# Kernel tuning notes

Hardware: AMD Instinct MI355X
Metric: run time of the kernel (lower is better)

The kernel has to match this reference:

```python
import jax, jax.numpy as jnp
import numpy as np

D_MODEL = 1024
NHEAD = 16
HEAD_DIM = D_MODEL // NHEAD
D_FF = 4096
BIAS_HID = 8
EPS = 1e-5


def _pair_bias(m, w1, b1, w2, b2):
    # m: [B,S,S] -> bias [B,S,S,nhead] via per-scalar MLP 1->hid->nhead
    h = jax.nn.relu(m[..., None] * w1 + b1)          # [B,S,S,hid]
    return jnp.einsum('bxyh,hn->bxyn', h, w2) + b2   # [B,S,S,nhead]


def _layernorm(x, g, b):
    mu = jnp.mean(x, axis=-1, keepdims=True)
    var = jnp.mean(jnp.square(x - mu), axis=-1, keepdims=True)
    return (x - mu) * jax.lax.rsqrt(var + EPS) * g + b


def setup_inputs() -> dict:
    key = jax.random.key(0)
    ks = jax.random.split(key, 20)
    B, S = 4, 1024
    sc = 1.0 / np.sqrt(D_MODEL)
    inp = {
        'src': jax.random.normal(ks[0], (B, S, D_MODEL), jnp.float32),
        't_deltas': jax.random.uniform(ks[1], (B, S, S), jnp.float32),
        'dists': jax.random.uniform(ks[2], (B, S, S), jnp.float32),
        'Wq': jax.random.normal(ks[3], (D_MODEL, D_MODEL), jnp.float32) * sc,
        'bq': jnp.zeros((D_MODEL,), jnp.float32),
        'Wk': jax.random.normal(ks[4], (D_MODEL, D_MODEL), jnp.float32) * sc,
        'bk': jnp.zeros((D_MODEL,), jnp.float32),
        'Wv': jax.random.normal(ks[5], (D_MODEL, D_MODEL), jnp.float32) * sc,
        'bv': jnp.zeros((D_MODEL,), jnp.float32),
        'tb_w1': jax.random.normal(ks[6], (BIAS_HID,), jnp.float32),
        'tb_b1': jnp.zeros((BIAS_HID,), jnp.float32),
        'tb_w2': jax.random.normal(ks[7], (BIAS_HID, NHEAD), jnp.float32) * 0.3,
        'tb_b2': jnp.zeros((NHEAD,), jnp.float32),
        'db_w1': jax.random.normal(ks[8], (BIAS_HID,), jnp.float32),
        'db_b1': jnp.zeros((BIAS_HID,), jnp.float32),
        'db_w2': jax.random.normal(ks[9], (BIAS_HID, NHEAD), jnp.float32) * 0.3,
        'db_b2': jnp.zeros((NHEAD,), jnp.float32),
        'W1': jax.random.normal(ks[10], (D_MODEL, D_FF), jnp.float32) * sc,
        'b1': jnp.zeros((D_FF,), jnp.float32),
        'W2': jax.random.normal(ks[11], (D_FF, D_MODEL), jnp.float32) / np.sqrt(D_FF),
        'b2': jnp.zeros((D_MODEL,), jnp.float32),
        'g1': jnp.ones((D_MODEL,), jnp.float32),
        'beta1': jnp.zeros((D_MODEL,), jnp.float32),
        'g2': jnp.ones((D_MODEL,), jnp.float32),
        'beta2': jnp.zeros((D_MODEL,), jnp.float32),
    }
    return inp


def reference(src, t_deltas, dists, Wq, bq, Wk, bk, Wv, bv,
              tb_w1, tb_b1, tb_w2, tb_b2, db_w1, db_b1, db_w2, db_b2,
              W1, b1, W2, b2, g1, beta1, g2, beta2):
    B, S, _ = src.shape
    # QKV projections -> [B, H, S, hd]
    q = (src @ Wq + bq).reshape(B, S, NHEAD, HEAD_DIM).transpose(0, 2, 1, 3)
    k = (src @ Wk + bk).reshape(B, S, NHEAD, HEAD_DIM).transpose(0, 2, 1, 3)
    v = (src @ Wv + bv).reshape(B, S, NHEAD, HEAD_DIM).transpose(0, 2, 1, 3)
    # scores scaled by sqrt(d_model) (as in the original, not head_dim)
    scores = jnp.einsum('bhqd,bhkd->bhqk', q, k) / jnp.sqrt(jnp.float32(D_MODEL))
    bias = (_pair_bias(t_deltas, tb_w1, tb_b1, tb_w2, tb_b2)
            + _pair_bias(dists, db_w1, db_b1, db_w2, db_b2))  # [B,S,S,H]
    scores = scores + bias.transpose(0, 3, 1, 2)
    attn = jax.nn.softmax(scores, axis=-1)
    out = jnp.einsum('bhqk,bhkd->bhqd', attn, v)
    out = out.transpose(0, 2, 1, 3).reshape(B, S, D_MODEL)
    x = _layernorm(src + out, g1, beta1)
    ffn = jax.nn.relu(x @ W1 + b1) @ W2 + b2
    return _layernorm(x + ffn, g2, beta2)
```

## Files before the change

### kernel.cpp

```cpp
#include <hip/hip_runtime.h>

typedef __bf16 bf16x8 __attribute__((ext_vector_type(8)));
typedef float f32x4 __attribute__((ext_vector_type(4)));
typedef unsigned short u16;

__device__ __forceinline__ u16 f2bf(float f) {
  union { float f; unsigned u; } x; x.f = f;
  unsigned r = x.u + 0x7fffu + ((x.u >> 16) & 1u);
  return (u16)(r >> 16);
}
__device__ __forceinline__ float bf2f(u16 u) {
  union { unsigned u; float f; } x; x.u = ((unsigned)u) << 16;
  return x.f;
}
__device__ __forceinline__ void gl_lds16(const void* g, void* l) {
  __builtin_amdgcn_global_load_lds(
      (const __attribute__((address_space(1))) void*)g,
      (__attribute__((address_space(3))) void*)l, 16, 0, 0);
}

__global__ __launch_bounds__(256) void cvt_kernel(const float* __restrict__ in,
                                                  u16* __restrict__ out, int n4) {
  int i = blockIdx.x * 256 + threadIdx.x;
  if (i >= n4) return;
  float4 v = ((const float4*)in)[i];
  unsigned lo = (unsigned)f2bf(v.x) | ((unsigned)f2bf(v.y) << 16);
  unsigned hi = (unsigned)f2bf(v.z) | ((unsigned)f2bf(v.w) << 16);
  uint2 u; u.x = lo; u.y = hi;
  *(uint2*)&out[(size_t)i * 4] = u;
}

__global__ __launch_bounds__(256) void tconv_kernel(const float* __restrict__ in,
                                                    u16* __restrict__ out, int R, int C) {
  __shared__ float tile[32][33];
  int c0 = blockIdx.x * 32, r0 = blockIdx.y * 32;
  int tx = threadIdx.x & 31, ty = threadIdx.x >> 5;
#pragma unroll
  for (int i = 0; i < 4; i++)
    tile[ty + i * 8][tx] = in[(size_t)(r0 + ty + i * 8) * C + c0 + tx];
  __syncthreads();
#pragma unroll
  for (int i = 0; i < 4; i++)
    out[(size_t)(c0 + ty + i * 8) * R + r0 + tx] = f2bf(tile[tx][ty + i * 8]);
}

__global__ __launch_bounds__(256) void bcat_kernel(const float* __restrict__ bq,
                                                   const float* __restrict__ bk,
                                                   const float* __restrict__ bv,
                                                   float* __restrict__ o) {
  int i = blockIdx.x * 256 + threadIdx.x;
  if (i >= 3072) return;
  o[i] = i < 1024 ? bq[i] : (i < 2048 ? bk[i - 1024] : bv[i - 2048]);
}

template <int EPI>
__global__ __launch_bounds__(256) void gemm128_kernel(const u16* __restrict__ A,
                                                      const u16* __restrict__ Bt,
                                                      const float* __restrict__ bias,
                                                      void* __restrict__ out,
                                                      int M, int N, int K,
                                                      float qscale, int kslice) {
  __shared__ u16 lds[2][2][2][4096];
  int tid = threadIdx.x, w = tid >> 6, lane = tid & 63;
  int l16 = lane & 15, lhi = lane >> 4;
  int wr = w >> 1, wc = w & 1;
  int GX = gridDim.x;
  int nwg = GX * gridDim.y;
  int nlin = blockIdx.y * GX + blockIdx.x;
  int cpx = nwg >> 3;
  int sw = (nlin & 7) * cpx + (nlin >> 3);
  int m0 = (sw / GX) * 128, n0 = (sw % GX) * 128;
  int z = blockIdx.z;
  const u16* Ag = A + (size_t)m0 * K + z * kslice;
  const u16* Bg = Bt + (size_t)n0 * K + z * kslice;
  f32x4 acc[4][4] = {};
  int nt = kslice >> 6;

  int srow = tid >> 2;
  int sxor = ((tid & 3) ^ ((tid >> 3) & 3)) * 8;
  int rga = (lhi ^ ((l16 >> 1) & 3)) * 8;

  auto stageTK = [&](int buf, int kh, int t) {
    const u16* As = Ag + (size_t)t * 64 + kh * 32 + sxor;
    const u16* Bs = Bg + (size_t)t * 64 + kh * 32 + sxor;
#pragma unroll
    for (int ld = 0; ld < 2; ld++)
      gl_lds16(As + (size_t)(ld * 64 + srow) * K, &lds[buf][0][kh][ld * 2048 + w * 512]);
#pragma unroll
    for (int ld = 0; ld < 2; ld++)
      gl_lds16(Bs + (size_t)(ld * 64 + srow) * K, &lds[buf][1][kh][ld * 2048 + w * 512]);
  };
  auto rdAB = [&](int buf, int kh, bf16x8 (&af)[4], bf16x8 (&bfr)[4]) {
#pragma unroll
    for (int m = 0; m < 4; m++)
      af[m] = *(const bf16x8*)&lds[buf][0][kh][(wr * 64 + m * 16 + l16) * 32 + rga];
#pragma unroll
    for (int nn = 0; nn < 4; nn++)
      bfr[nn] = *(const bf16x8*)&lds[buf][1][kh][(wc * 64 + nn * 16 + l16) * 32 + rga];
  };
  auto mma16 = [&](bf16x8 (&af)[4], bf16x8 (&bfr)[4]) {
    __builtin_amdgcn_s_setprio(1);
#pragma unroll
    for (int m = 0; m < 4; m++)
#pragma unroll
      for (int nn = 0; nn < 4; nn++)
        acc[m][nn] =
            __builtin_amdgcn_mfma_f32_16x16x32_bf16(af[m], bfr[nn], acc[m][nn], 0, 0, 0);
    __builtin_amdgcn_s_setprio(0);
  };

  stageTK(0, 0, 0);
  stageTK(0, 1, 0);
  stageTK(1, 0, 1);

  for (int t = 0; t < nt; ++t) {
    int buf = t & 1, bufn = buf ^ 1;
    bool last = (t == nt - 1);
    bf16x8 af[4], bfr[4];
    if (!last) asm volatile("s_waitcnt vmcnt(8)" ::: "memory");
    else       asm volatile("s_waitcnt vmcnt(4)" ::: "memory");
    __builtin_amdgcn_s_barrier();
    rdAB(buf, 0, af, bfr);
    if (t + 1 < nt) stageTK(bufn, 1, t + 1);
    asm volatile("s_waitcnt lgkmcnt(0)" ::: "memory");
    __builtin_amdgcn_sched_barrier(0);
    mma16(af, bfr);
    if (!last) asm volatile("s_waitcnt vmcnt(8)" ::: "memory");
    else       asm volatile("s_waitcnt vmcnt(0)" ::: "memory");
    __builtin_amdgcn_s_barrier();
    rdAB(buf, 1, af, bfr);
    if (t + 2 < nt) stageTK(buf, 0, t + 2);
    asm volatile("s_waitcnt lgkmcnt(0)" ::: "memory");
    __builtin_amdgcn_sched_barrier(0);
    mma16(af, bfr);
  }

#pragma unroll
  for (int m = 0; m < 4; m++) {
    int gr = m0 + wr * 64 + m * 16 + lhi * 4;
#pragma unroll
    for (int nn = 0; nn < 4; nn++) {
      int gc = n0 + wc * 64 + nn * 16 + l16;
      float bv;
      if (EPI == 0 || EPI == 3) bv = (z == 0 && bias) ? bias[gc] : 0.f;
      else bv = bias[gc];
      if (EPI == 2) {
        int seg = gc >> 10, c = gc & 1023, h = c >> 6, d = c & 63;
        float sc = (seg == 0) ? qscale : 1.f;
#pragma unroll
        for (int r = 0; r < 4; r++) {
          int row = gr + r;
          int b = row >> 10, s = row & 1023;
          size_t idx = ((((size_t)seg * 4 + b) * 16 + h) * 1024 + s) * 64 + d;
          ((u16*)out)[idx] = f2bf((acc[m][nn][r] + bv) * sc);
        }
      } else if (EPI == 1) {
#pragma unroll
        for (int r = 0; r < 4; r++)
          ((u16*)out)[(size_t)(gr + r) * N + gc] = f2bf(fmaxf(acc[m][nn][r] + bv, 0.f));
      } else if (EPI == 3) {
#pragma unroll
        for (int r = 0; r < 4; r++)
          ((u16*)out)[(size_t)z * M * N + (size_t)(gr + r) * N + gc] = f2bf(acc[m][nn][r] + bv);
      } else {
#pragma unroll
        for (int r = 0; r < 4; r++)
          ((float*)out)[(size_t)z * M * N + (size_t)(gr + r) * N + gc] = acc[m][nn][r] + bv;
      }
    }
  }
}

__global__ __launch_bounds__(256) void vtrans_kernel(const u16* __restrict__ v,
                                                     u16* __restrict__ vt) {
  __shared__ u16 t[64][72];
  int bh = blockIdx.y, s0 = blockIdx.x * 64;
  int tid = threadIdx.x;
  int r = tid >> 2, c = (tid & 3) * 16;
  const u16* src = v + ((size_t)bh * 1024 + s0 + r) * 64 + c;
  *(int4*)&t[r][c] = *(const int4*)src;
  *(int4*)&t[r][c + 8] = *(const int4*)(src + 8);
  __syncthreads();
  int d = tid >> 2, sc = (tid & 3) * 16;
  u16 tmp[16];
#pragma unroll
  for (int j = 0; j < 16; j++) tmp[j] = t[sc + j][d];
  u16* dst = vt + ((size_t)bh * 64 + d) * 1024 + s0 + sc;
  *(int4*)dst = *(int4*)&tmp[0];
  *(int4*)(dst + 8) = *(int4*)&tmp[8];
}

__global__ __launch_bounds__(256) void bias_kernel(
    const float* __restrict__ td, const float* __restrict__ dd,
    const float* __restrict__ tw1, const float* __restrict__ tb1,
    const float* __restrict__ tw2, const float* __restrict__ tb2,
    const float* __restrict__ dw1, const float* __restrict__ db1,
    const float* __restrict__ dw2, const float* __restrict__ db2,
    u16* __restrict__ biasout, int b0) {
  __shared__ float stw2[128], sdw2[128], sb2[16];
  __shared__ float stw1[8], stb1[8], sdw1[8], sdb1[8];
  int tid = threadIdx.x, x = blockIdx.x, bz = blockIdx.y;
  int b = b0 + bz;
  if (tid < 128) { stw2[tid] = tw2[tid]; sdw2[tid] = dw2[tid]; }
  if (tid < 16) sb2[tid] = tb2[tid] + db2[tid];
  if (tid < 8) { stw1[tid] = tw1[tid]; stb1[tid] = tb1[tid]; sdw1[tid] = dw1[tid]; sdb1[tid] = db1[tid]; }
  __syncthreads();
  float4 tv = ((const float4*)(td + ((size_t)b * 1024 + x) * 1024))[tid];
  float4 dv = ((const float4*)(dd + ((size_t)b * 1024 + x) * 1024))[tid];
  float tj[4] = {tv.x, tv.y, tv.z, tv.w};
  float dj[4] = {dv.x, dv.y, dv.z, dv.w};
  float ht[4][8], hd[4][8];
#pragma unroll
  for (int j = 0; j < 4; j++)
#pragma unroll
    for (int i = 0; i < 8; i++) {
      ht[j][i] = fmaxf(tj[j] * stw1[i] + stb1[i], 0.f);
      hd[j][i] = fmaxf(dj[j] * sdw1[i] + sdb1[i], 0.f);
    }
  u16* outb = biasout + (size_t)bz * 16 * 1024 * 1024 + (size_t)x * 1024 + tid * 4;
#pragma unroll
  for (int h = 0; h < 16; h++) {
    float a[4];
#pragma unroll
    for (int j = 0; j < 4; j++) {
      float s = sb2[h];
#pragma unroll
      for (int i = 0; i < 8; i++)
        s += ht[j][i] * stw2[i * 16 + h] + hd[j][i] * sdw2[i * 16 + h];
      a[j] = s;
    }
    unsigned lo = (unsigned)f2bf(a[0]) | ((unsigned)f2bf(a[1]) << 16);
    unsigned hi = (unsigned)f2bf(a[2]) | ((unsigned)f2bf(a[3]) << 16);
    uint2 u; u.x = lo; u.y = hi;
    *(uint2*)&outb[(size_t)h * 1024 * 1024] = u;
  }
}

#define LDA 72
__global__ __launch_bounds__(256) void attn_kernel(
    const u16* __restrict__ qg, const u16* __restrict__ kg, const u16* __restrict__ vtg,
    const u16* __restrict__ bias, float* __restrict__ attn_out, int b0) {
  __shared__ u16 Ks[64 * LDA];
  __shared__ u16 Vt[64 * LDA];
  __shared__ u16 Ps[64 * LDA];
  int tid = threadIdx.x;
  int w = tid >> 6, l = tid & 63, l16 = l & 15, lhi = l >> 4;
  int qt = blockIdx.x, h = blockIdx.y, bz = blockIdx.z;
  int b = b0 + bz;
  size_t bh = ((size_t)(b * 16 + h)) * 1024 * 64;
  const u16* biasb = bias + (size_t)bz * 16 * 1024 * 1024 + (size_t)h * 1024 * 1024;
  int qrow = qt * 64 + w * 16 + l16;
  bf16x8 qa[2];
  qa[0] = *(const bf16x8*)&qg[bh + (size_t)qrow * 64 + lhi * 8];
  qa[1] = *(const bf16x8*)&qg[bh + (size_t)qrow * 64 + 32 + lhi * 8];

  float m_run[4], l_run[4];
  f32x4 o[4] = {};
#pragma unroll
  for (int r = 0; r < 4; r++) { m_run[r] = -1e30f; l_run[r] = 0.f; }

  int kr0 = (tid * 2) >> 3, kc0 = ((tid * 2) & 7) * 8;
  int kr1 = (tid * 2 + 1) >> 3, kc1 = ((tid * 2 + 1) & 7) * 8;
  const u16* kbase = kg + bh;
  const u16* vbase = vtg + bh;

  int4 kA, kB, vA, vB;
  u16 bpre[16];
  auto issueKV = [&](int kt) {
    kA = *(const int4*)&kbase[(size_t)(kt * 64 + kr0) * 64 + kc0];
    kB = *(const int4*)&kbase[(size_t)(kt * 64 + kr1) * 64 + kc1];
    vA = *(const int4*)&vbase[(size_t)kr0 * 1024 + kt * 64 + kc0];
    vB = *(const int4*)&vbase[(size_t)kr1 * 1024 + kt * 64 + kc1];
  };
  auto issueBias = [&](int kt) {
#pragma unroll
    for (int ni = 0; ni < 4; ni++)
#pragma unroll
      for (int r = 0; r < 4; r++)
        bpre[ni * 4 + r] =
            biasb[(size_t)(qt * 64 + w * 16 + lhi * 4 + r) * 1024 + kt * 64 + ni * 16 + l16];
  };
  issueKV(0);
  issueBias(0);

  for (int kt = 0; kt < 16; kt++) {
    __syncthreads();
    *(int4*)&Ks[kr0 * LDA + kc0] = kA;
    *(int4*)&Ks[kr1 * LDA + kc1] = kB;
    *(int4*)&Vt[kr0 * LDA + kc0] = vA;
    *(int4*)&Vt[kr1 * LDA + kc1] = vB;
    __syncthreads();
    u16 bcur[16];
#pragma unroll
    for (int i = 0; i < 16; i++) bcur[i] = bpre[i];
    if (kt + 1 < 16) { issueKV(kt + 1); issueBias(kt + 1); }
    __builtin_amdgcn_sched_barrier(0);

    f32x4 s[4] = {};
    __builtin_amdgcn_s_setprio(1);
#pragma unroll
    for (int ni = 0; ni < 4; ni++)
#pragma unroll
      for (int ks = 0; ks < 2; ks++) {
        bf16x8 kb = *(const bf16x8*)&Ks[(ni * 16 + l16) * LDA + ks * 32 + lhi * 8];
        s[ni] = __builtin_amdgcn_mfma_f32_16x16x32_bf16(qa[ks], kb, s[ni], 0, 0, 0);
      }
    __builtin_amdgcn_s_setprio(0);
#pragma unroll
    for (int ni = 0; ni < 4; ni++)
#pragma unroll
      for (int r = 0; r < 4; r++)
        s[ni][r] += bf2f(bcur[ni * 4 + r]);
    float rs[4];
#pragma unroll
    for (int r = 0; r < 4; r++) {
      float m = fmaxf(fmaxf(s[0][r], s[1][r]), fmaxf(s[2][r], s[3][r]));
      m = fmaxf(m, __shfl_xor(m, 1, 16));
      m = fmaxf(m, __shfl_xor(m, 2, 16));
      m = fmaxf(m, __shfl_xor(m, 4, 16));
      m = fmaxf(m, __shfl_xor(m, 8, 16));
      float m2 = fmaxf(m_run[r], m);
      float sc = __expf(m_run[r] - m2);
      float sum = 0.f;
#pragma unroll
      for (int ni = 0; ni < 4; ni++) {
        float p = __expf(s[ni][r] - m2);
        s[ni][r] = p;
        sum += p;
      }
      sum += __shfl_xor(sum, 1, 16);
      sum += __shfl_xor(sum, 2, 16);
      sum += __shfl_xor(sum, 4, 16);
      sum += __shfl_xor(sum, 8, 16);
      l_run[r] = l_run[r] * sc + sum;
      m_run[r] = m2;
      rs[r] = sc;
    }
#pragma unroll
    for (int di = 0; di < 4; di++)
#pragma unroll
      for (int r = 0; r < 4; r++)
        o[di][r] *= rs[r];
#pragma unroll
    for (int ni = 0; ni < 4; ni++)
#pragma unroll
      for (int r = 0; r < 4; r++)
        Ps[(w * 16 + lhi * 4 + r) * LDA + ni * 16 + l16] = f2bf(s[ni][r]);
    __builtin_amdgcn_s_setprio(1);
#pragma unroll
    for (int ks = 0; ks < 2; ks++) {
      bf16x8 pa = *(const bf16x8*)&Ps[(w * 16 + l16) * LDA + ks * 32 + lhi * 8];
#pragma unroll
      for (int di = 0; di < 4; di++) {
        bf16x8 vb = *(const bf16x8*)&Vt[(di * 16 + l16) * LDA + ks * 32 + lhi * 8];
        o[di] = __builtin_amdgcn_mfma_f32_16x16x32_bf16(pa, vb, o[di], 0, 0, 0);
      }
    }
    __builtin_amdgcn_s_setprio(0);
  }
#pragma unroll
  for (int r = 0; r < 4; r++) {
    float inv = 1.f / l_run[r];
    int row = b * 1024 + qt * 64 + w * 16 + lhi * 4 + r;
#pragma unroll
    for (int di = 0; di < 4; di++)
      attn_out[(size_t)row * 1024 + h * 64 + di * 16 + l16] = o[di][r] * inv;
  }
}

__global__ __launch_bounds__(256) void ln_kernel(const float* __restrict__ a,
                                                 const float* __restrict__ r1,
                                                 const float* __restrict__ g,
                                                 const float* __restrict__ beta,
                                                 float* __restrict__ outf,
                                                 u16* __restrict__ outbf) {
  int row = blockIdx.x, tid = threadIdx.x;
  __shared__ float red[8];
  float4 va = ((const float4*)(a + (size_t)row * 1024))[tid];
  float4 vr = ((const float4*)(r1 + (size_t)row * 1024))[tid];
  float v[4] = {va.x + vr.x, va.y + vr.y, va.z + vr.z, va.w + vr.w};
  float s = v[0] + v[1] + v[2] + v[3];
#pragma unroll
  for (int off = 32; off >= 1; off >>= 1) s += __shfl_xor(s, off, 64);
  if ((tid & 63) == 0) red[tid >> 6] = s;
  __syncthreads();
  float mean = (red[0] + red[1] + red[2] + red[3]) * (1.f / 1024.f);
  float q = 0.f;
#pragma unroll
  for (int j = 0; j < 4; j++) { float d = v[j] - mean; q += d * d; }
#pragma unroll
  for (int off = 32; off >= 1; off >>= 1) q += __shfl_xor(q, off, 64);
  if ((tid & 63) == 0) red[4 + (tid >> 6)] = q;
  __syncthreads();
  float var = (red[4] + red[5] + red[6] + red[7]) * (1.f / 1024.f);
  float rstd = rsqrtf(var + 1e-5f);
  float4 gv = ((const float4*)g)[tid];
  float4 bv = ((const float4*)beta)[tid];
  float o0 = (v[0] - mean) * rstd * gv.x + bv.x;
  float o1 = (v[1] - mean) * rstd * gv.y + bv.y;
  float o2 = (v[2] - mean) * rstd * gv.z + bv.z;
  float o3 = (v[3] - mean) * rstd * gv.w + bv.w;
  float4 ov; ov.x = o0; ov.y = o1; ov.z = o2; ov.w = o3;
  ((float4*)(outf + (size_t)row * 1024))[tid] = ov;
  unsigned lo = (unsigned)f2bf(o0) | ((unsigned)f2bf(o1) << 16);
  unsigned hi = (unsigned)f2bf(o2) | ((unsigned)f2bf(o3) << 16);
  uint2 u; u.x = lo; u.y = hi;
  *(uint2*)&outbf[(size_t)row * 1024 + tid * 4] = u;
}

__global__ __launch_bounds__(256) void ln2_kernel(const float* __restrict__ x,
                                                  const u16* __restrict__ ff, int zs,
                                                  const float* __restrict__ g,
                                                  const float* __restrict__ beta,
                                                  float* __restrict__ out) {
  int row = blockIdx.x, tid = threadIdx.x;
  __shared__ float red[8];
  float4 xv = ((const float4*)(x + (size_t)row * 1024))[tid];
  float v[4] = {xv.x, xv.y, xv.z, xv.w};
  for (int z = 0; z < zs; z++) {
    uint2 u = *(const uint2*)&ff[(size_t)z * 4096 * 1024 + (size_t)row * 1024 + tid * 4];
    v[0] += bf2f(u.x & 0xffff); v[1] += bf2f(u.x >> 16);
    v[2] += bf2f(u.y & 0xffff); v[3] += bf2f(u.y >> 16);
  }
  float s = v[0] + v[1] + v[2] + v[3];
#pragma unroll
  for (int off = 32; off >= 1; off >>= 1) s += __shfl_xor(s, off, 64);
  if ((tid & 63) == 0) red[tid >> 6] = s;
  __syncthreads();
  float mean = (red[0] + red[1] + red[2] + red[3]) * (1.f / 1024.f);
  float q = 0.f;
#pragma unroll
  for (int j = 0; j < 4; j++) { float d = v[j] - mean; q += d * d; }
#pragma unroll
  for (int off = 32; off >= 1; off >>= 1) q += __shfl_xor(q, off, 64);
  if ((tid & 63) == 0) red[4 + (tid >> 6)] = q;
  __syncthreads();
  float var = (red[4] + red[5] + red[6] + red[7]) * (1.f / 1024.f);
  float rstd = rsqrtf(var + 1e-5f);
  float4 gv = ((const float4*)g)[tid];
  float4 bv = ((const float4*)beta)[tid];
  float4 ov;
  ov.x = (v[0] - mean) * rstd * gv.x + bv.x;
  ov.y = (v[1] - mean) * rstd * gv.y + bv.y;
  ov.z = (v[2] - mean) * rstd * gv.z + bv.z;
  ov.w = (v[3] - mean) * rstd * gv.w + bv.w;
  ((float4*)(out + (size_t)row * 1024))[tid] = ov;
}

extern "C" void kernel_launch(void* const* d_in, const int* in_sizes, int n_in,
                              void* d_out, int out_size, void* d_ws, size_t ws_size,
                              hipStream_t stream) {
  const float* src      = (const float*)d_in[0];
  const float* t_deltas = (const float*)d_in[1];
  const float* dists    = (const float*)d_in[2];
  const float* Wq = (const float*)d_in[3];
  const float* bq = (const float*)d_in[4];
  const float* Wk = (const float*)d_in[5];
  const float* bk = (const float*)d_in[6];
  const float* Wv = (const float*)d_in[7];
  const float* bv = (const float*)d_in[8];
  const float* tb_w1 = (const float*)d_in[9];
  const float* tb_b1 = (const float*)d_in[10];
  const float* tb_w2 = (const float*)d_in[11];
  const float* tb_b2 = (const float*)d_in[12];
  const float* db_w1 = (const float*)d_in[13];
  const float* db_b1 = (const float*)d_in[14];
  const float* db_w2 = (const float*)d_in[15];
  const float* db_b2 = (const float*)d_in[16];
  const float* W1 = (const float*)d_in[17];
  const float* b1 = (const float*)d_in[18];
  const float* W2 = (const float*)d_in[19];
  const float* b2 = (const float*)d_in[20];
  const float* g1 = (const float*)d_in[21];
  const float* beta1 = (const float*)d_in[22];
  const float* g2 = (const float*)d_in[23];
  const float* beta2 = (const float*)d_in[24];
  float* out = (float*)d_out;

  const size_t MB = 1024u * 1024;
  bool big = ws_size >= 150 * MB;
  int PB = big ? 2 : 1;
  int ZS = big ? 4 : 2;

  char* ws = (char*)d_ws;
  size_t off = 0;
  auto alloc = [&](size_t n) { void* p = ws + off; off += (n + 255) & ~(size_t)255; return p; };
  u16* src_bf  = (u16*)alloc(4096u * 1024 * 2);
  u16* wqkv_bt = (u16*)alloc(3072u * 1024 * 2);
  u16* w1_bt   = (u16*)alloc(4096u * 1024 * 2);
  u16* w2_bt   = (u16*)alloc(1024u * 4096 * 2);
  float* bcat  = (float*)alloc(3072u * 4);
  u16* qkv     = (u16*)alloc(3u * 4 * 16 * 1024 * 64 * 2);
  u16* vt      = (u16*)alloc(4u * 16 * 64 * 1024 * 2);
  u16* slab    = (u16*)alloc((size_t)PB * 16 * 1024 * 1024 * 2);
  float* attn_out = (float*)alloc(4096u * 1024 * 4);
  (void)in_sizes; (void)n_in; (void)out_size;

  u16* q_bf = qkv;
  u16* k_bf = qkv + 4u * 16 * 1024 * 64;
  u16* v_bf = qkv + 8u * 16 * 1024 * 64;
  float* x_f32 = (float*)qkv;
  u16*   x_bf  = (u16*)((char*)qkv + 16 * MB);
  u16*   h_bf  = (u16*)vt;
  u16*   ffnb  = big ? (u16*)((char*)slab + 24 * MB)
                     : (u16*)attn_out;

  cvt_kernel<<<4096, 256, 0, stream>>>(src, src_bf, 4096 * 1024 / 4);
  tconv_kernel<<<dim3(32, 32), 256, 0, stream>>>(Wq, wqkv_bt, 1024, 1024);
  tconv_kernel<<<dim3(32, 32), 256, 0, stream>>>(Wk, wqkv_bt + 1024u * 1024, 1024, 1024);
  tconv_kernel<<<dim3(32, 32), 256, 0, stream>>>(Wv, wqkv_bt + 2048u * 1024, 1024, 1024);
  tconv_kernel<<<dim3(128, 32), 256, 0, stream>>>(W1, w1_bt, 1024, 4096);
  tconv_kernel<<<dim3(32, 128), 256, 0, stream>>>(W2, w2_bt, 4096, 1024);
  bcat_kernel<<<12, 256, 0, stream>>>(bq, bk, bv, bcat);

  gemm128_kernel<2><<<dim3(24, 32, 1), 256, 0, stream>>>(src_bf, wqkv_bt, bcat, qkv,
                                                         4096, 3072, 1024, 1.f / 32.f, 1024);
  vtrans_kernel<<<dim3(16, 64), 256, 0, stream>>>(v_bf, vt);

  for (int p = 0; p < 4 / PB; p++) {
    bias_kernel<<<dim3(1024, PB), 256, 0, stream>>>(t_deltas, dists, tb_w1, tb_b1, tb_w2, tb_b2,
                                                    db_w1, db_b1, db_w2, db_b2, slab, p * PB);
    attn_kernel<<<dim3(16, 16, PB), 256, 0, stream>>>(q_bf, k_bf, vt, slab, attn_out, p * PB);
  }

  ln_kernel<<<4096, 256, 0, stream>>>(src, attn_out, g1, beta1, x_f32, x_bf);
  gemm128_kernel<1><<<dim3(32, 32, 1), 256, 0, stream>>>(x_bf, w1_bt, b1, h_bf,
                                                         4096, 4096, 1024, 1.f, 1024);
  gemm128_kernel<3><<<dim3(8, 32, ZS), 256, 0, stream>>>(h_bf, w2_bt, b2, ffnb,
                                                         4096, 1024, 4096, 1.f, 4096 / ZS);
  ln2_kernel<<<4096, 256, 0, stream>>>(x_f32, ffnb, ZS, g2, beta2, out);
}
```

Before: 308.9 us.

## Load K/V fragments directly from global in attention, drop LDS staging

```diff
diff --git a/kernel.cpp b/kernel.cpp
--- a/kernel.cpp
+++ b/kernel.cpp
@@ -240,8 +240,6 @@
 __global__ __launch_bounds__(256) void attn_kernel(
     const u16* __restrict__ qg, const u16* __restrict__ kg, const u16* __restrict__ vtg,
     const u16* __restrict__ bias, float* __restrict__ attn_out, int b0) {
-  __shared__ u16 Ks[64 * LDA];
-  __shared__ u16 Vt[64 * LDA];
   __shared__ u16 Ps[64 * LDA];
   int tid = threadIdx.x;
   int w = tid >> 6, l = tid & 63, l16 = l & 15, lhi = l >> 4;
@@ -259,19 +257,10 @@
 #pragma unroll
   for (int r = 0; r < 4; r++) { m_run[r] = -1e30f; l_run[r] = 0.f; }
 
-  int kr0 = (tid * 2) >> 3, kc0 = ((tid * 2) & 7) * 8;
-  int kr1 = (tid * 2 + 1) >> 3, kc1 = ((tid * 2 + 1) & 7) * 8;
   const u16* kbase = kg + bh;
   const u16* vbase = vtg + bh;
 
-  int4 kA, kB, vA, vB;
   u16 bpre[16];
-  auto issueKV = [&](int kt) {
-    kA = *(const int4*)&kbase[(size_t)(kt * 64 + kr0) * 64 + kc0];
-    kB = *(const int4*)&kbase[(size_t)(kt * 64 + kr1) * 64 + kc1];
-    vA = *(const int4*)&vbase[(size_t)kr0 * 1024 + kt * 64 + kc0];
-    vB = *(const int4*)&vbase[(size_t)kr1 * 1024 + kt * 64 + kc1];
-  };
   auto issueBias = [&](int kt) {
 #pragma unroll
     for (int ni = 0; ni < 4; ni++)
@@ -280,21 +269,13 @@
         bpre[ni * 4 + r] =
             biasb[(size_t)(qt * 64 + w * 16 + lhi * 4 + r) * 1024 + kt * 64 + ni * 16 + l16];
   };
-  issueKV(0);
   issueBias(0);
 
   for (int kt = 0; kt < 16; kt++) {
-    __syncthreads();
-    *(int4*)&Ks[kr0 * LDA + kc0] = kA;
-    *(int4*)&Ks[kr1 * LDA + kc1] = kB;
-    *(int4*)&Vt[kr0 * LDA + kc0] = vA;
-    *(int4*)&Vt[kr1 * LDA + kc1] = vB;
-    __syncthreads();
     u16 bcur[16];
 #pragma unroll
     for (int i = 0; i < 16; i++) bcur[i] = bpre[i];
-    if (kt + 1 < 16) { issueKV(kt + 1); issueBias(kt + 1); }
-    __builtin_amdgcn_sched_barrier(0);
+    if (kt + 1 < 16) issueBias(kt + 1);
 
     f32x4 s[4] = {};
     __builtin_amdgcn_s_setprio(1);
@@ -302,7 +283,8 @@
     for (int ni = 0; ni < 4; ni++)
 #pragma unroll
       for (int ks = 0; ks < 2; ks++) {
-        bf16x8 kb = *(const bf16x8*)&Ks[(ni * 16 + l16) * LDA + ks * 32 + lhi * 8];
+        bf16x8 kb =
+            *(const bf16x8*)&kbase[(size_t)(kt * 64 + ni * 16 + l16) * 64 + ks * 32 + lhi * 8];
         s[ni] = __builtin_amdgcn_mfma_f32_16x16x32_bf16(qa[ks], kb, s[ni], 0, 0, 0);
       }
     __builtin_amdgcn_s_setprio(0);
@@ -352,7 +334,8 @@
       bf16x8 pa = *(const bf16x8*)&Ps[(w * 16 + l16) * LDA + ks * 32 + lhi * 8];
 #pragma unroll
       for (int di = 0; di < 4; di++) {
-        bf16x8 vb = *(const bf16x8*)&Vt[(di * 16 + l16) * LDA + ks * 32 + lhi * 8];
+        bf16x8 vb =
+            *(const bf16x8*)&vbase[(size_t)(di * 16 + l16) * 1024 + kt * 64 + ks * 32 + lhi * 8];
         o[di] = __builtin_amdgcn_mfma_f32_16x16x32_bf16(pa, vb, o[di], 0, 0, 0);
       }
     }
@@ -480,7 +463,7 @@
   const size_t MB = 1024u * 1024;
   bool big = ws_size >= 150 * MB;
   int PB = big ? 2 : 1;
-  int ZS = big ? 4 : 2;
+  const int ZS = 2;
 
   char* ws = (char*)d_ws;
   size_t off = 0;
@@ -502,8 +485,7 @@
   float* x_f32 = (float*)qkv;
   u16*   x_bf  = (u16*)((char*)qkv + 16 * MB);
   u16*   h_bf  = (u16*)vt;
-  u16*   ffnb  = big ? (u16*)((char*)slab + 24 * MB)
-                     : (u16*)attn_out;
+  u16*   ffnb  = (u16*)attn_out;
 
   cvt_kernel<<<4096, 256, 0, stream>>>(src, src_bf, 4096 * 1024 / 4);
   tconv_kernel<<<dim3(32, 32), 256, 0, stream>>>(Wq, wqkv_bt, 1024, 1024);
```

Measured after the change: 365.0 us. +18.2%, slower.
